# Kernel tuning notes

Measured on AMD Instinct MI355X. Metric: run time of the kernel, lower is better.

The kernel has to match this reference:

```python
import jax, jax.numpy as jnp
import numpy as np

BN_EPS = 1e-5

def conv1x1(x, w, b):
    # x: [B,C,H,W], w: [O,C], b: [O] -> [B,O,H,W]
    return jnp.einsum('bchw,oc->bohw', x, w) + b[None, :, None, None]

def setup_inputs() -> dict:
    key = jax.random.key(0)
    ks = jax.random.split(key, 12)
    B, C, H, W = 16, 512, 64, 32
    Ch = C // 2  # hidden_channel
    s = 0.02
    return {
        'x':       jax.random.normal(ks[0], (B, C, H, W), jnp.float32),
        'theta_w': jax.random.normal(ks[1], (Ch, C), jnp.float32) * s,
        'theta_b': jax.random.normal(ks[2], (Ch,), jnp.float32) * s,
        'phi_w':   jax.random.normal(ks[3], (Ch, C), jnp.float32) * s,
        'phi_b':   jax.random.normal(ks[4], (Ch,), jnp.float32) * s,
        'g_w':     jax.random.normal(ks[5], (Ch, C), jnp.float32) * s,
        'g_b':     jax.random.normal(ks[6], (Ch,), jnp.float32) * s,
        'W_w':     jax.random.normal(ks[7], (C, Ch), jnp.float32) * s,
        'W_b':     jax.random.normal(ks[8], (C,), jnp.float32) * s,
        'bn_gamma': 1.0 + jax.random.normal(ks[9], (C,), jnp.float32) * 0.1,
        'bn_beta':  jax.random.normal(ks[10], (C,), jnp.float32) * 0.1,
    }

def reference(x, theta_w, theta_b, phi_w, phi_b, g_w, g_b, W_w, W_b, bn_gamma, bn_beta):
    B, C, H, Wd = x.shape
    N = H * Wd
    Ch = theta_w.shape[0]
    # 1x1 conv projections, flattened over spatial dims
    th = conv1x1(x, theta_w, theta_b).reshape(B, Ch, N)  # theta: [B,Ch,N]
    ph = conv1x1(x, phi_w, phi_b).reshape(B, Ch, N)      # phi:   [B,Ch,N]
    gv = conv1x1(x, g_w, g_b).reshape(B, Ch, N)          # g:     [B,Ch,N]
    # dense affinity (no softmax), normalized by N, as in the original
    f = jnp.einsum('bcn,bcm->bnm', th, ph) / N           # [B,N,N]
    y = jnp.einsum('bnm,bcm->bcn', f, gv).reshape(B, Ch, H, Wd)
    # W: 1x1 conv + BatchNorm2d (training-mode batch statistics, biased var)
    w = conv1x1(y, W_w, W_b)                             # [B,C,H,W]
    mean = w.mean(axis=(0, 2, 3), keepdims=True)
    var = w.var(axis=(0, 2, 3), keepdims=True)
    wn = (w - mean) * jax.lax.rsqrt(var + BN_EPS)
    wn = wn * bn_gamma[None, :, None, None] + bn_beta[None, :, None, None]
    return wn + x
```

## Files before the change

kernel.cpp:

```cpp
#include <hip/hip_runtime.h>

typedef __bf16 bf16x8 __attribute__((ext_vector_type(8)));
typedef float floatx4 __attribute__((ext_vector_type(4)));

#define DEVI __device__ __forceinline__

DEVI unsigned short f2bf(float f) {
  union { float f; unsigned u; } v; v.f = f;
  unsigned r = v.u + 0x7FFFu + ((v.u >> 16) & 1u);
  return (unsigned short)(r >> 16);
}

DEVI void gload_lds16(const void* g, void* l) {
  __builtin_amdgcn_global_load_lds((const __attribute__((address_space(1))) void*)g,
                                   (__attribute__((address_space(3))) void*)l,
                                   16, 0, 0);
}

__global__ __launch_bounds__(256) void k_transpose(
    const float* __restrict__ x, unsigned short* __restrict__ xt,
    const float* __restrict__ phi_w, const float* __restrict__ g_w,
    const float* __restrict__ theta_w, const float* __restrict__ W_w,
    const float* __restrict__ phi_b, const float* __restrict__ g_b,
    unsigned short* __restrict__ wpg, unsigned short* __restrict__ thw,
    unsigned short* __restrict__ ww, float* __restrict__ pgbias) {
  const int t = threadIdx.x;
  if (blockIdx.z == 16) {
    const int T0 = 512 * 512, T1 = T0 + 256 * 512, T2 = T1 + 512 * 256, T3 = T2 + 512;
    int base = (blockIdx.y * 32 + blockIdx.x) * 256 + t;
    for (int i = base; i < T3; i += 65536) {
      if (i < T0) {
        int o = i >> 9, c = i & 511;
        float v = (o < 256) ? phi_w[o * 512 + c] : g_w[(o - 256) * 512 + c];
        wpg[i] = f2bf(v);
      } else if (i < T1) {
        int j = i - T0; thw[j] = f2bf(theta_w[j]);
      } else if (i < T2) {
        int j = i - T1; ww[j] = f2bf(W_w[j]);
      } else {
        int o = i - T2; pgbias[o] = (o < 256) ? phi_b[o] : g_b[o - 256];
      }
    }
    return;
  }
  __shared__ float tile[64][65];
  const int b = blockIdx.z, c0 = blockIdx.y * 64, n0 = blockIdx.x * 64;
  const float* xb = x + (size_t)b * 512 * 2048;
#pragma unroll
  for (int i = 0; i < 16; ++i) {
    int lin = i * 256 + t;
    int lc = lin >> 6, ln = lin & 63;
    tile[lc][ln] = xb[(size_t)(c0 + lc) * 2048 + (n0 + ln)];
  }
  __syncthreads();
  unsigned short* xtb = xt + (size_t)b * 2048 * 512;
#pragma unroll
  for (int i = 0; i < 16; ++i) {
    int lin = i * 256 + t;
    int ln = lin >> 6, lc = lin & 63;
    xtb[(size_t)(n0 + ln) * 512 + (c0 + lc)] = f2bf(tile[lc][ln]);
  }
}

template <int BM, int BN, int EPI>
__global__ __launch_bounds__(256) void k_gemm(
    const unsigned short* __restrict__ A, const unsigned short* __restrict__ B,
    unsigned short* __restrict__ C, int N, int K,
    size_t sA, size_t sB, size_t sC,
    const float* __restrict__ bias, float scale) {
  constexpr int WM = BM / 2, WN = BN / 2;
  constexpr int FM = WM / 16, FN = WN / 16;
  __shared__ __align__(16) __bf16 At[BM * 64];
  __shared__ __align__(16) __bf16 Bt[BN * 64];
  const int t = threadIdx.x;
  const int z = blockIdx.z;
  const int row0 = blockIdx.y * BM, col0 = blockIdx.x * BN;
  const unsigned short* Az = A + (size_t)z * sA;
  const unsigned short* Bz = B + (size_t)z * sB;
  unsigned short* Cz = C + (size_t)z * sC;

  const int w = t >> 6, lane = t & 63;
  const int l16 = lane & 15, lq = lane >> 4;
  const int wrow0 = (w >> 1) * WM, wcol0 = (w & 1) * WN;
  const int xorb = (l16 & 7) << 4;
  const int aoff0 = (wrow0 + l16) * 128;
  const int boff0 = (wcol0 + l16) * 128;

  floatx4 acc[FM][FN];
#pragma unroll
  for (int m = 0; m < FM; ++m)
#pragma unroll
    for (int n = 0; n < FN; ++n) acc[m][n] = (floatx4){0.f, 0.f, 0.f, 0.f};

  const int kt_end = K >> 6;
  for (int kt = 0; kt < kt_end; ++kt) {
    __syncthreads();
#pragma unroll
    for (int i = 0; i < BM * 8 / 256; ++i) {
      int ch = i * 256 + t;
      int r = ch >> 3;
      int sc = ((((ch & 7) << 4) ^ ((r & 7) << 4)) >> 1);
      gload_lds16(Az + (size_t)(row0 + r) * K + (kt << 6) + sc, &At[ch * 8]);
    }
#pragma unroll
    for (int i = 0; i < BN * 8 / 256; ++i) {
      int ch = i * 256 + t;
      int r = ch >> 3;
      int sc = ((((ch & 7) << 4) ^ ((r & 7) << 4)) >> 1);
      gload_lds16(Bz + (size_t)(col0 + r) * K + (kt << 6) + sc, &Bt[ch * 8]);
    }
    __syncthreads();

#pragma unroll
    for (int kk = 0; kk < 2; ++kk) {
      const int ck = ((kk << 6) + (lq << 4)) ^ xorb;
      bf16x8 af[FM], bq[FN];
#pragma unroll
      for (int m = 0; m < FM; ++m)
        af[m] = *(const bf16x8*)((const char*)At + aoff0 + m * 2048 + ck);
#pragma unroll
      for (int n = 0; n < FN; ++n)
        bq[n] = *(const bf16x8*)((const char*)Bt + boff0 + n * 2048 + ck);
#pragma unroll
      for (int m = 0; m < FM; ++m)
#pragma unroll
        for (int n = 0; n < FN; ++n)
          acc[m][n] = __builtin_amdgcn_mfma_f32_16x16x32_bf16(af[m], bq[n], acc[m][n], 0, 0, 0);
    }
  }

#pragma unroll
  for (int m = 0; m < FM; ++m)
#pragma unroll
    for (int n = 0; n < FN; ++n) {
      int gc = col0 + wcol0 + n * 16 + l16;
      float bc = (EPI == 2) ? bias[gc] : 0.f;
#pragma unroll
      for (int r = 0; r < 4; ++r) {
        int gr = row0 + wrow0 + m * 16 + lq * 4 + r;
        float v = acc[m][n][r] * scale;
        if (EPI == 1) v += bias[gr];
        if (EPI == 2) v += bc;
        Cz[(size_t)gr * N + gc] = f2bf(v);
      }
    }
}

__global__ __launch_bounds__(512) void k_gemm_splitk(const unsigned short* __restrict__ phg,
                                                     float* __restrict__ amatf) {
  __shared__ __align__(16) __bf16 At[256 * 64];
  __shared__ __align__(16) __bf16 Bt[256 * 64];
  const int t = threadIdx.x;
  const int split = blockIdx.x, b = blockIdx.z;
  const size_t sPG = (size_t)512 * 2048;
  const unsigned short* Az = phg + (size_t)b * sPG;
  const unsigned short* Bz = Az + (size_t)256 * 2048;
  const int w = t >> 6, lane = t & 63;
  const int l16 = lane & 15, lq = lane >> 4;
  const int wrow0 = (w >> 2) * 128, wcol0 = (w & 3) * 64;
  const int xorb = (l16 & 7) << 4;
  const int aoff0 = (wrow0 + l16) * 128;
  const int boff0 = (wcol0 + l16) * 128;

  floatx4 acc[8][4];
#pragma unroll
  for (int m = 0; m < 8; ++m)
#pragma unroll
    for (int n = 0; n < 4; ++n) acc[m][n] = (floatx4){0.f, 0.f, 0.f, 0.f};

#pragma unroll
  for (int ks = 0; ks < 2; ++ks) {
    const int kt = split * 2 + ks;
    __syncthreads();
#pragma unroll
    for (int i = 0; i < 4; ++i) {
      int ch = i * 512 + t;
      int r = ch >> 3;
      int sc = ((((ch & 7) << 4) ^ ((r & 7) << 4)) >> 1);
      gload_lds16(Az + (size_t)r * 2048 + (kt << 6) + sc, &At[ch * 8]);
    }
#pragma unroll
    for (int i = 0; i < 4; ++i) {
      int ch = i * 512 + t;
      int r = ch >> 3;
      int sc = ((((ch & 7) << 4) ^ ((r & 7) << 4)) >> 1);
      gload_lds16(Bz + (size_t)r * 2048 + (kt << 6) + sc, &Bt[ch * 8]);
    }
    __syncthreads();
#pragma unroll
    for (int kk = 0; kk < 2; ++kk) {
      const int ck = ((kk << 6) + (lq << 4)) ^ xorb;
      bf16x8 af[8], bq[4];
#pragma unroll
      for (int m = 0; m < 8; ++m)
        af[m] = *(const bf16x8*)((const char*)At + aoff0 + m * 2048 + ck);
#pragma unroll
      for (int n = 0; n < 4; ++n)
        bq[n] = *(const bf16x8*)((const char*)Bt + boff0 + n * 2048 + ck);
#pragma unroll
      for (int m = 0; m < 8; ++m)
#pragma unroll
        for (int n = 0; n < 4; ++n)
          acc[m][n] = __builtin_amdgcn_mfma_f32_16x16x32_bf16(af[m], bq[n], acc[m][n], 0, 0, 0);
    }
  }
  float* out = amatf + (size_t)b * 256 * 256;
#pragma unroll
  for (int m = 0; m < 8; ++m)
#pragma unroll
    for (int n = 0; n < 4; ++n)
#pragma unroll
      for (int r = 0; r < 4; ++r) {
        int gr = wrow0 + m * 16 + lq * 4 + r;
        int gc = wcol0 + n * 16 + l16;
        unsafeAtomicAdd(&out[gr * 256 + gc], acc[m][n][r]);
      }
}

__global__ __launch_bounds__(256) void k_gemm_f32b(const unsigned short* __restrict__ ww,
                                                   const float* __restrict__ amatf,
                                                   unsigned short* __restrict__ mmat) {
  __shared__ __align__(16) __bf16 At[64 * 32];
  __shared__ __align__(16) __bf16 Bt[64 * 32];
  const int t = threadIdx.x;
  const int b = blockIdx.z;
  const int col0 = blockIdx.x * 64;
  const int row0 = blockIdx.y * 64;
  const float* Bz = amatf + (size_t)b * 256 * 256;
  const int w = t >> 6, lane = t & 63;
  const int l16 = lane & 15, lq = lane >> 4;
  const int wrow0 = (w >> 1) * 32, wcol0 = (w & 1) * 32;

  floatx4 acc[2][2];
#pragma unroll
  for (int m = 0; m < 2; ++m)
#pragma unroll
    for (int n = 0; n < 2; ++n) acc[m][n] = (floatx4){0.f, 0.f, 0.f, 0.f};

  for (int kt = 0; kt < 8; ++kt) {
    __syncthreads();
    {
      int r = t >> 2, kq = t & 3;
      gload_lds16(ww + (size_t)(row0 + r) * 256 + (kt << 5) + (kq << 3), &At[t * 8]);
    }
    {
      int r = t >> 2, kq = t & 3;
      const float* src = Bz + (size_t)(col0 + r) * 256 + (kt << 5) + (kq << 3);
      float4 a = *(const float4*)src;
      float4 c = *(const float4*)(src + 4);
      union { unsigned short s[8]; bf16x8 v; } pk;
      pk.s[0] = f2bf(a.x); pk.s[1] = f2bf(a.y); pk.s[2] = f2bf(a.z); pk.s[3] = f2bf(a.w);
      pk.s[4] = f2bf(c.x); pk.s[5] = f2bf(c.y); pk.s[6] = f2bf(c.z); pk.s[7] = f2bf(c.w);
      *(bf16x8*)&Bt[t * 8] = pk.v;
    }
    __syncthreads();
    bf16x8 af[2], bq[2];
#pragma unroll
    for (int m = 0; m < 2; ++m)
      af[m] = *(const bf16x8*)&At[(wrow0 + m * 16 + l16) * 32 + lq * 8];
#pragma unroll
    for (int n = 0; n < 2; ++n)
      bq[n] = *(const bf16x8*)&Bt[(wcol0 + n * 16 + l16) * 32 + lq * 8];
#pragma unroll
    for (int m = 0; m < 2; ++m)
#pragma unroll
      for (int n = 0; n < 2; ++n)
        acc[m][n] = __builtin_amdgcn_mfma_f32_16x16x32_bf16(af[m], bq[n], acc[m][n], 0, 0, 0);
  }
  unsigned short* Cz = mmat + (size_t)b * 512 * 256;
  const float scale = 1.f / 2048.f;
#pragma unroll
  for (int m = 0; m < 2; ++m)
#pragma unroll
    for (int n = 0; n < 2; ++n)
#pragma unroll
      for (int r = 0; r < 4; ++r) {
        int gr = row0 + wrow0 + m * 16 + lq * 4 + r;
        int gc = col0 + wcol0 + n * 16 + l16;
        Cz[(size_t)gr * 256 + gc] = f2bf(acc[m][n][r] * scale);
      }
}

__global__ __launch_bounds__(256) void k_bnstats(const unsigned short* __restrict__ w,
                                                 const float* __restrict__ gamma,
                                                 const float* __restrict__ beta,
                                                 float* __restrict__ scale,
                                                 float* __restrict__ shift) {
  const int c = blockIdx.x, t = threadIdx.x;
  float s = 0.f, ss = 0.f;
  for (int b = 0; b < 16; ++b) {
    const unsigned short* p = w + ((size_t)b * 512 + c) * 2048 + t * 8;
    uint4 v = *(const uint4*)p;
    unsigned u[4] = {v.x, v.y, v.z, v.w};
#pragma unroll
    for (int j = 0; j < 4; ++j) {
      union { unsigned q; float f; } a, bb;
      a.q = u[j] << 16;
      bb.q = u[j] & 0xFFFF0000u;
      s += a.f + bb.f;
      ss += a.f * a.f + bb.f * bb.f;
    }
  }
#pragma unroll
  for (int off = 32; off; off >>= 1) {
    s += __shfl_down(s, off);
    ss += __shfl_down(ss, off);
  }
  __shared__ float ls[4], lss[4];
  if ((t & 63) == 0) { ls[t >> 6] = s; lss[t >> 6] = ss; }
  __syncthreads();
  if (t == 0) {
    float S = ls[0] + ls[1] + ls[2] + ls[3];
    float SS = lss[0] + lss[1] + lss[2] + lss[3];
    const float inv = 1.f / 32768.f;
    float mean = S * inv;
    float var = SS * inv - mean * mean;
    float rs = rsqrtf(var + 1e-5f);
    float sc = gamma[c] * rs;
    scale[c] = sc;
    shift[c] = beta[c] - mean * sc;
  }
}

__global__ __launch_bounds__(256) void k_final(const unsigned short* __restrict__ w,
                                               const float* __restrict__ x,
                                               const float* __restrict__ scale,
                                               const float* __restrict__ shift,
                                               float* __restrict__ out) {
  const size_t total4 = (size_t)16 * 512 * 2048 / 4;
  size_t stride = (size_t)gridDim.x * 256;
  for (size_t i = (size_t)blockIdx.x * 256 + threadIdx.x; i < total4; i += stride) {
    size_t e = i * 4;
    int c = (int)((e >> 11) & 511);
    float sc = scale[c], sh = shift[c];
    uint2 wv = *(const uint2*)(w + e);
    float4 xv = *(const float4*)(x + e);
    float4 o;
    union { unsigned q; float f; } a;
    a.q = wv.x << 16;          o.x = a.f * sc + sh + xv.x;
    a.q = wv.x & 0xFFFF0000u;  o.y = a.f * sc + sh + xv.y;
    a.q = wv.y << 16;          o.z = a.f * sc + sh + xv.z;
    a.q = wv.y & 0xFFFF0000u;  o.w = a.f * sc + sh + xv.w;
    *(float4*)(out + e) = o;
  }
}

extern "C" void kernel_launch(void* const* d_in, const int* in_sizes, int n_in,
                              void* d_out, int out_size, void* d_ws, size_t ws_size,
                              hipStream_t stream) {
  const float* x       = (const float*)d_in[0];
  const float* theta_w = (const float*)d_in[1];
  const float* theta_b = (const float*)d_in[2];
  const float* phi_w   = (const float*)d_in[3];
  const float* phi_b   = (const float*)d_in[4];
  const float* g_w     = (const float*)d_in[5];
  const float* g_b     = (const float*)d_in[6];
  const float* W_w     = (const float*)d_in[7];
  const float* W_b     = (const float*)d_in[8];
  const float* gamma   = (const float*)d_in[9];
  const float* beta    = (const float*)d_in[10];
  float* out = (float*)d_out;

  char* ws = (char*)d_ws;
  size_t off = 0;
  auto alloc = [&](size_t bytes) {
    char* p = ws + off;
    off = (off + bytes + 255) & ~(size_t)255;
    return p;
  };
  unsigned short* xt    = (unsigned short*)alloc((size_t)16 * 2048 * 512 * 2);
  unsigned short* phg   = (unsigned short*)alloc((size_t)16 * 512 * 2048 * 2);
  unsigned short* tht   = (unsigned short*)alloc((size_t)16 * 2048 * 256 * 2);
  float*          amatf = (float*)alloc((size_t)16 * 256 * 256 * 4);
  unsigned short* mmat  = (unsigned short*)alloc((size_t)16 * 512 * 256 * 2);
  unsigned short* wbuf  = (unsigned short*)alloc((size_t)16 * 512 * 2048 * 2);
  unsigned short* wpg   = (unsigned short*)alloc((size_t)512 * 512 * 2);
  unsigned short* thw   = (unsigned short*)alloc((size_t)256 * 512 * 2);
  unsigned short* ww    = (unsigned short*)alloc((size_t)512 * 256 * 2);
  float* pgbias         = (float*)alloc(512 * 4);
  float* scalev         = (float*)alloc(512 * 4);
  float* shiftv         = (float*)alloc(512 * 4);
  (void)ws_size; (void)in_sizes; (void)n_in; (void)out_size;

  const size_t sXT = (size_t)2048 * 512;
  const size_t sPG = (size_t)512 * 2048;
  const size_t sTH = (size_t)2048 * 256;
  const size_t sMM = (size_t)512 * 256;
  const size_t sW  = (size_t)512 * 2048;

  hipMemsetAsync(amatf, 0, (size_t)16 * 256 * 256 * 4, stream);

  k_transpose<<<dim3(32, 8, 17), 256, 0, stream>>>(x, xt, phi_w, g_w, theta_w, W_w,
                                                   phi_b, g_b, wpg, thw, ww, pgbias);

  k_gemm<128, 128, 1><<<dim3(16, 4, 16), 256, 0, stream>>>(
      wpg, xt, phg, 2048, 512, 0, sXT, sPG, pgbias, 1.f);
  k_gemm<128, 128, 2><<<dim3(2, 16, 16), 256, 0, stream>>>(
      xt, thw, tht, 256, 512, sXT, 0, sTH, theta_b, 1.f);
  k_gemm_splitk<<<dim3(16, 1, 16), 512, 0, stream>>>(phg, amatf);
  k_gemm_f32b<<<dim3(4, 8, 16), 256, 0, stream>>>(ww, amatf, mmat);
  k_gemm<128, 128, 1><<<dim3(16, 4, 16), 256, 0, stream>>>(
      mmat, tht, wbuf, 2048, 256, sMM, sTH, sW, W_b, 1.f);

  k_bnstats<<<512, 256, 0, stream>>>(wbuf, gamma, beta, scalev, shiftv);
  k_final<<<4096, 256, 0, stream>>>(wbuf, x, scalev, shiftv, out);
}
```

Measured before the change: 290.8 us.

## Replace atomic split-K with partial buffers reduced in the consumer GEMM

The phi·g^T split-K GEMM used to run 16 splits of 256x256 tiles per batch and combine them with float atomics into a buffer that was zeroed first. It now uses 4 K-splits times 4 output tiles of 128x128 with 256 threads, and writes plain stores into a 4-way partial buffer. The following GEMM sums the four partials while loading. This removes the memset and the atomic traffic, at the cost of more workspace memory and extra partial reads in the next kernel.

```diff
diff --git a/kernel.cpp b/kernel.cpp
--- a/kernel.cpp
+++ b/kernel.cpp
@@ -146,42 +146,43 @@
     }
 }
 
-__global__ __launch_bounds__(512) void k_gemm_splitk(const unsigned short* __restrict__ phg,
-                                                     float* __restrict__ amatf) {
-  __shared__ __align__(16) __bf16 At[256 * 64];
-  __shared__ __align__(16) __bf16 Bt[256 * 64];
+__global__ __launch_bounds__(256) void k_gemm_part(const unsigned short* __restrict__ phg,
+                                                   float* __restrict__ pbuf) {
+  __shared__ __align__(16) __bf16 At[128 * 64];
+  __shared__ __align__(16) __bf16 Bt[128 * 64];
   const int t = threadIdx.x;
-  const int split = blockIdx.x, b = blockIdx.z;
+  const int tid = blockIdx.x, b = blockIdx.z;
+  const int split = tid >> 2, tr = (tid >> 1) & 1, tc = tid & 1;
+  const int row0 = tr * 128, col0 = tc * 128;
   const size_t sPG = (size_t)512 * 2048;
-  const unsigned short* Az = phg + (size_t)b * sPG;
-  const unsigned short* Bz = Az + (size_t)256 * 2048;
+  const unsigned short* Az = phg + (size_t)b * sPG + (size_t)row0 * 2048;
+  const unsigned short* Bz = phg + (size_t)b * sPG + (size_t)(256 + col0) * 2048;
   const int w = t >> 6, lane = t & 63;
   const int l16 = lane & 15, lq = lane >> 4;
-  const int wrow0 = (w >> 2) * 128, wcol0 = (w & 3) * 64;
+  const int wrow0 = (w >> 1) * 64, wcol0 = (w & 1) * 64;
   const int xorb = (l16 & 7) << 4;
   const int aoff0 = (wrow0 + l16) * 128;
   const int boff0 = (wcol0 + l16) * 128;
 
-  floatx4 acc[8][4];
-#pragma unroll
-  for (int m = 0; m < 8; ++m)
+  floatx4 acc[4][4];
+#pragma unroll
+  for (int m = 0; m < 4; ++m)
 #pragma unroll
     for (int n = 0; n < 4; ++n) acc[m][n] = (floatx4){0.f, 0.f, 0.f, 0.f};
 
-#pragma unroll
-  for (int ks = 0; ks < 2; ++ks) {
-    const int kt = split * 2 + ks;
+  for (int kt8 = 0; kt8 < 8; ++kt8) {
+    const int kt = split * 8 + kt8;
     __syncthreads();
 #pragma unroll
     for (int i = 0; i < 4; ++i) {
-      int ch = i * 512 + t;
+      int ch = i * 256 + t;
       int r = ch >> 3;
       int sc = ((((ch & 7) << 4) ^ ((r & 7) << 4)) >> 1);
       gload_lds16(Az + (size_t)r * 2048 + (kt << 6) + sc, &At[ch * 8]);
     }
 #pragma unroll
     for (int i = 0; i < 4; ++i) {
-      int ch = i * 512 + t;
+      int ch = i * 256 + t;
       int r = ch >> 3;
       int sc = ((((ch & 7) << 4) ^ ((r & 7) << 4)) >> 1);
       gload_lds16(Bz + (size_t)r * 2048 + (kt << 6) + sc, &Bt[ch * 8]);
@@ -190,35 +191,35 @@
 #pragma unroll
     for (int kk = 0; kk < 2; ++kk) {
       const int ck = ((kk << 6) + (lq << 4)) ^ xorb;
-      bf16x8 af[8], bq[4];
-#pragma unroll
-      for (int m = 0; m < 8; ++m)
+      bf16x8 af[4], bq[4];
+#pragma unroll
+      for (int m = 0; m < 4; ++m)
         af[m] = *(const bf16x8*)((const char*)At + aoff0 + m * 2048 + ck);
 #pragma unroll
       for (int n = 0; n < 4; ++n)
         bq[n] = *(const bf16x8*)((const char*)Bt + boff0 + n * 2048 + ck);
 #pragma unroll
-      for (int m = 0; m < 8; ++m)
+      for (int m = 0; m < 4; ++m)
 #pragma unroll
         for (int n = 0; n < 4; ++n)
           acc[m][n] = __builtin_amdgcn_mfma_f32_16x16x32_bf16(af[m], bq[n], acc[m][n], 0, 0, 0);
     }
   }
-  float* out = amatf + (size_t)b * 256 * 256;
-#pragma unroll
-  for (int m = 0; m < 8; ++m)
+  float* outp = pbuf + ((size_t)split * 16 + b) * 65536;
+#pragma unroll
+  for (int m = 0; m < 4; ++m)
 #pragma unroll
     for (int n = 0; n < 4; ++n)
 #pragma unroll
       for (int r = 0; r < 4; ++r) {
-        int gr = wrow0 + m * 16 + lq * 4 + r;
-        int gc = wcol0 + n * 16 + l16;
-        unsafeAtomicAdd(&out[gr * 256 + gc], acc[m][n][r]);
+        int gr = row0 + wrow0 + m * 16 + lq * 4 + r;
+        int gc = col0 + wcol0 + n * 16 + l16;
+        outp[(size_t)gr * 256 + gc] = acc[m][n][r];
       }
 }
 
 __global__ __launch_bounds__(256) void k_gemm_f32b(const unsigned short* __restrict__ ww,
-                                                   const float* __restrict__ amatf,
+                                                   const float* __restrict__ pbuf,
                                                    unsigned short* __restrict__ mmat) {
   __shared__ __align__(16) __bf16 At[64 * 32];
   __shared__ __align__(16) __bf16 Bt[64 * 32];
@@ -226,7 +227,8 @@
   const int b = blockIdx.z;
   const int col0 = blockIdx.x * 64;
   const int row0 = blockIdx.y * 64;
-  const float* Bz = amatf + (size_t)b * 256 * 256;
+  const size_t SSTR = (size_t)16 * 65536;
+  const float* Bz = pbuf + (size_t)b * 65536;
   const int w = t >> 6, lane = t & 63;
   const int l16 = lane & 15, lq = lane >> 4;
   const int wrow0 = (w >> 1) * 32, wcol0 = (w & 1) * 32;
@@ -248,6 +250,13 @@
       const float* src = Bz + (size_t)(col0 + r) * 256 + (kt << 5) + (kq << 3);
       float4 a = *(const float4*)src;
       float4 c = *(const float4*)(src + 4);
+#pragma unroll
+      for (int s = 1; s < 4; ++s) {
+        float4 a2 = *(const float4*)(src + s * SSTR);
+        float4 c2 = *(const float4*)(src + s * SSTR + 4);
+        a.x += a2.x; a.y += a2.y; a.z += a2.z; a.w += a2.w;
+        c.x += c2.x; c.y += c2.y; c.z += c2.z; c.w += c2.w;
+      }
       union { unsigned short s[8]; bf16x8 v; } pk;
       pk.s[0] = f2bf(a.x); pk.s[1] = f2bf(a.y); pk.s[2] = f2bf(a.z); pk.s[3] = f2bf(a.w);
       pk.s[4] = f2bf(c.x); pk.s[5] = f2bf(c.y); pk.s[6] = f2bf(c.z); pk.s[7] = f2bf(c.w);
@@ -371,7 +380,7 @@
   unsigned short* xt    = (unsigned short*)alloc((size_t)16 * 2048 * 512 * 2);
   unsigned short* phg   = (unsigned short*)alloc((size_t)16 * 512 * 2048 * 2);
   unsigned short* tht   = (unsigned short*)alloc((size_t)16 * 2048 * 256 * 2);
-  float*          amatf = (float*)alloc((size_t)16 * 256 * 256 * 4);
+  float*          pbuf  = (float*)alloc((size_t)4 * 16 * 256 * 256 * 4);
   unsigned short* mmat  = (unsigned short*)alloc((size_t)16 * 512 * 256 * 2);
   unsigned short* wbuf  = (unsigned short*)alloc((size_t)16 * 512 * 2048 * 2);
   unsigned short* wpg   = (unsigned short*)alloc((size_t)512 * 512 * 2);
@@ -388,8 +397,6 @@
   const size_t sMM = (size_t)512 * 256;
   const size_t sW  = (size_t)512 * 2048;
 
-  hipMemsetAsync(amatf, 0, (size_t)16 * 256 * 256 * 4, stream);
-
   k_transpose<<<dim3(32, 8, 17), 256, 0, stream>>>(x, xt, phi_w, g_w, theta_w, W_w,
                                                    phi_b, g_b, wpg, thw, ww, pgbias);
 
@@ -397,8 +404,8 @@
       wpg, xt, phg, 2048, 512, 0, sXT, sPG, pgbias, 1.f);
   k_gemm<128, 128, 2><<<dim3(2, 16, 16), 256, 0, stream>>>(
       xt, thw, tht, 256, 512, sXT, 0, sTH, theta_b, 1.f);
-  k_gemm_splitk<<<dim3(16, 1, 16), 512, 0, stream>>>(phg, amatf);
-  k_gemm_f32b<<<dim3(4, 8, 16), 256, 0, stream>>>(ww, amatf, mmat);
+  k_gemm_part<<<dim3(16, 1, 16), 256, 0, stream>>>(phg, pbuf);
+  k_gemm_f32b<<<dim3(4, 8, 16), 256, 0, stream>>>(ww, pbuf, mmat);
   k_gemm<128, 128, 1><<<dim3(16, 4, 16), 256, 0, stream>>>(
       mmat, tht, wbuf, 2048, 256, sMM, sTH, sW, W_b, 1.f);
 
```

Result: faster. 253.1 us (-13.0%).
